# Optimization experiments

Hardware: AMD Instinct MI355X
Metric: run time of the kernel (lower is better)

Reference implementation:

```python
import jax, jax.numpy as jnp
import numpy as np

A_LO, A_HI = -1.0, 1.0  # arbitrary_range


def _kbit_gaussian(q_lo: float, q_hi: float, n_bit: int) -> jnp.ndarray:
    # torch: norm.ppf of quantiles 1/n..(n-1)/n, cast to fp16, then affine-normalize in fp16
    p = jnp.arange(1, n_bit, dtype=jnp.float32) / n_bit
    v = jax.scipy.stats.norm.ppf(p).astype(jnp.float16)
    return q_lo + (v - v[0]) / (v[-1] - v[0]) * (q_hi - q_lo)


def make_codebook() -> jnp.ndarray:
    neg = _kbit_gaussian(A_LO, 0.0, 2 ** 3)            # 7 values in [-1, 0]
    pos = _kbit_gaussian(0.0, A_HI, 2 ** 3 + 1)[1:]     # 8 values in (0, 1]
    return jnp.concatenate([neg, pos])                  # [15], float16


def setup_inputs() -> dict:
    key = jax.random.key(0)
    x = jax.random.normal(key, (2048, 4096), dtype=jnp.float32)
    codebook = make_codebook()
    return {"x": x, "codebook": codebook}


def reference(x, codebook):
    # fit: global min/max
    x_min = jnp.min(x)
    x_max = jnp.max(x)
    # fit_transform: clamp (no-op at fit min/max) + affine map to [A_LO, A_HI]
    x_norm = (jnp.clip(x, x_min, x_max) - x_min) / (x_max - x_min) * (A_HI - A_LO) + A_LO
    # nearest-codebook lookup: |x - c| argmin over 15-entry codebook, then gather
    dist = jnp.abs(x_norm[..., None] - codebook)  # [..., 15] (fp32, codebook upcast as in torch)
    idx = jnp.argmin(dist, axis=-1)
    return codebook[idx]  # float16, same shape as x
```

## Files before the change

### kernel.cpp

```cpp
#include <hip/hip_runtime.h>
#include <hip/hip_fp16.h>
#include <float.h>

#define N_CB 15
#define A_BLOCKS 512
#define A_THREADS 256
#define B_THREADS 256


__global__ __launch_bounds__(A_THREADS) void q4_partials_kernel(
        const float4* __restrict__ x4, int n4,
        const float* __restrict__ x, int n,
        float* __restrict__ ws, const void* __restrict__ cb_raw) {
    if (blockIdx.x == 0 && threadIdx.x < N_CB) {
        const float* cf = (const float*)cb_raw;
        float v;
        if (cf[0] == -1.0f) v = cf[threadIdx.x];
        else                v = __half2float(((const __half*)cb_raw)[threadIdx.x]);
        ws[1024 + threadIdx.x] = v;
    }

    float mn = FLT_MAX, mx = -FLT_MAX;
    int tid = blockIdx.x * A_THREADS + threadIdx.x;
    int stride = gridDim.x * A_THREADS;
    for (int i = tid; i < n4; i += stride) {
        float4 v = x4[i];
        mn = fminf(mn, fminf(fminf(v.x, v.y), fminf(v.z, v.w)));
        mx = fmaxf(mx, fmaxf(fmaxf(v.x, v.y), fmaxf(v.z, v.w)));
    }
    if (blockIdx.x == 0) {
        for (int i = n4 * 4 + threadIdx.x; i < n; i += A_THREADS) {
            float v = x[i];
            mn = fminf(mn, v);
            mx = fmaxf(mx, v);
        }
    }
    #pragma unroll
    for (int off = 32; off; off >>= 1) {
        mn = fminf(mn, __shfl_down(mn, off));
        mx = fmaxf(mx, __shfl_down(mx, off));
    }
    __shared__ float smn[4], smx[4];
    int wave = threadIdx.x >> 6, lane = threadIdx.x & 63;
    if (lane == 0) { smn[wave] = mn; smx[wave] = mx; }
    __syncthreads();
    if (threadIdx.x == 0) {
        ws[blockIdx.x]       = fminf(fminf(smn[0], smn[1]), fminf(smn[2], smn[3]));
        ws[512 + blockIdx.x] = fmaxf(fmaxf(smx[0], smx[1]), fmaxf(smx[2], smx[3]));
    }
}

__device__ __forceinline__ float q4_lookup(float xv, float mn, float range,
                                           const float* cb) {
    float t = (xv - mn) / range * 2.0f - 1.0f;
    float best = fabsf(t - cb[0]);
    float val  = cb[0];
    #pragma unroll
    for (int j = 1; j < N_CB; j++) {
        float d = fabsf(t - cb[j]);
        if (d < best) { best = d; val = cb[j]; }
    }
    return val;
}

__global__ __launch_bounds__(B_THREADS) void q4_transform_kernel(
        const float4* __restrict__ x4, float4* __restrict__ out4, int n4,
        const float* __restrict__ x, float* __restrict__ out, int n,
        const float* __restrict__ ws) {
    int base = blockIdx.x * (B_THREADS * 2) + threadIdx.x;
    bool h0 = base < n4, h1 = (base + B_THREADS) < n4;
    float4 v0, v1;
    if (h0) v0 = x4[base];
    if (h1) v1 = x4[base + B_THREADS];

    float mn = fminf(ws[threadIdx.x],       ws[threadIdx.x + 256]);
    float mx = fmaxf(ws[512 + threadIdx.x], ws[768 + threadIdx.x]);
    #pragma unroll
    for (int off = 32; off; off >>= 1) {
        mn = fminf(mn, __shfl_down(mn, off));
        mx = fmaxf(mx, __shfl_down(mx, off));
    }
    __shared__ float sred[8];
    __shared__ float sfin[2];
    int wave = threadIdx.x >> 6, lane = threadIdx.x & 63;
    if (lane == 0) { sred[wave] = mn; sred[4 + wave] = mx; }
    __syncthreads();
    if (threadIdx.x == 0) {
        sfin[0] = fminf(fminf(sred[0], sred[1]), fminf(sred[2], sred[3]));
        sfin[1] = fmaxf(fmaxf(sred[4], sred[5]), fmaxf(sred[6], sred[7]));
    }
    float cb[N_CB];
    #pragma unroll
    for (int j = 0; j < N_CB; j++) cb[j] = ws[1024 + j];
    __syncthreads();
    float fmn = sfin[0];
    float range = sfin[1] - fmn;

    if (h0) {
        float4 o;
        o.x = q4_lookup(v0.x, fmn, range, cb);
        o.y = q4_lookup(v0.y, fmn, range, cb);
        o.z = q4_lookup(v0.z, fmn, range, cb);
        o.w = q4_lookup(v0.w, fmn, range, cb);
        out4[base] = o;
    }
    if (h1) {
        float4 o;
        o.x = q4_lookup(v1.x, fmn, range, cb);
        o.y = q4_lookup(v1.y, fmn, range, cb);
        o.z = q4_lookup(v1.z, fmn, range, cb);
        o.w = q4_lookup(v1.w, fmn, range, cb);
        out4[base + B_THREADS] = o;
    }
    if (blockIdx.x == 0) {
        for (int k = n4 * 4 + threadIdx.x; k < n; k += B_THREADS) {
            out[k] = q4_lookup(x[k], fmn, range, cb);
        }
    }
}

extern "C" void kernel_launch(void* const* d_in, const int* in_sizes, int n_in,
                              void* d_out, int out_size, void* d_ws, size_t ws_size,
                              hipStream_t stream) {
    const float* x = (const float*)d_in[0];
    const void* cb = d_in[1];
    float* out = (float*)d_out;
    int n = in_sizes[0];
    int n4 = n >> 2;
    float* ws = (float*)d_ws;

    q4_partials_kernel<<<A_BLOCKS, A_THREADS, 0, stream>>>(
        (const float4*)x, n4, x, n, ws, cb);

    int bblocks = (n4 + B_THREADS * 2 - 1) / (B_THREADS * 2);
    q4_transform_kernel<<<bblocks, B_THREADS, 0, stream>>>(
        (const float4*)x, (float4*)out, n4, x, out, n, ws);
}
```

Measured before the change: 97.32 us.

## Fuse min/max reduction and quantize into one cooperative kernel with register-held tiles

Replaces the two-kernel flow (partial min/max, then transform) with a single cooperative persistent kernel. Each thread loads up to eight float4 values into registers, does the min/max reduction, meets the other blocks at a grid-wide sync, and then quantizes the values it already holds. This removes the second full read of x and one kernel launch. In exchange it adds a grid.sync, uses more registers per thread, and depends on cooperative launch support, with the old two-kernel path kept as a fallback.

```diff
diff --git a/kernel.cpp b/kernel.cpp
--- a/kernel.cpp
+++ b/kernel.cpp
@@ -1,54 +1,15 @@
 #include <hip/hip_runtime.h>
 #include <hip/hip_fp16.h>
+#include <hip/hip_cooperative_groups.h>
 #include <float.h>
 
-#define N_CB 15
-#define A_BLOCKS 512
-#define A_THREADS 256
-#define B_THREADS 256
-
-
-__global__ __launch_bounds__(A_THREADS) void q4_partials_kernel(
-        const float4* __restrict__ x4, int n4,
-        const float* __restrict__ x, int n,
-        float* __restrict__ ws, const void* __restrict__ cb_raw) {
-    if (blockIdx.x == 0 && threadIdx.x < N_CB) {
-        const float* cf = (const float*)cb_raw;
-        float v;
-        if (cf[0] == -1.0f) v = cf[threadIdx.x];
-        else                v = __half2float(((const __half*)cb_raw)[threadIdx.x]);
-        ws[1024 + threadIdx.x] = v;
-    }
-
-    float mn = FLT_MAX, mx = -FLT_MAX;
-    int tid = blockIdx.x * A_THREADS + threadIdx.x;
-    int stride = gridDim.x * A_THREADS;
-    for (int i = tid; i < n4; i += stride) {
-        float4 v = x4[i];
-        mn = fminf(mn, fminf(fminf(v.x, v.y), fminf(v.z, v.w)));
-        mx = fmaxf(mx, fmaxf(fmaxf(v.x, v.y), fmaxf(v.z, v.w)));
-    }
-    if (blockIdx.x == 0) {
-        for (int i = n4 * 4 + threadIdx.x; i < n; i += A_THREADS) {
-            float v = x[i];
-            mn = fminf(mn, v);
-            mx = fmaxf(mx, v);
-        }
-    }
-    #pragma unroll
-    for (int off = 32; off; off >>= 1) {
-        mn = fminf(mn, __shfl_down(mn, off));
-        mx = fmaxf(mx, __shfl_down(mx, off));
-    }
-    __shared__ float smn[4], smx[4];
-    int wave = threadIdx.x >> 6, lane = threadIdx.x & 63;
-    if (lane == 0) { smn[wave] = mn; smx[wave] = mx; }
-    __syncthreads();
-    if (threadIdx.x == 0) {
-        ws[blockIdx.x]       = fminf(fminf(smn[0], smn[1]), fminf(smn[2], smn[3]));
-        ws[512 + blockIdx.x] = fmaxf(fmaxf(smx[0], smx[1]), fmaxf(smx[2], smx[3]));
-    }
-}
+namespace cg = cooperative_groups;
+
+#define N_CB  15
+#define MAXB  1024
+#define NTHR  256
+#define VPT   8
+
 
 __device__ __forceinline__ float q4_lookup(float xv, float mn, float range,
                                            const float* cb) {
@@ -63,18 +24,170 @@
     return val;
 }
 
-__global__ __launch_bounds__(B_THREADS) void q4_transform_kernel(
+__device__ __forceinline__ void q4_load_cb(const void* __restrict__ cb_raw, float* cb) {
+    const float* cf = (const float*)cb_raw;
+    if (cf[0] == -1.0f) {
+        #pragma unroll
+        for (int j = 0; j < N_CB; j++) cb[j] = cf[j];
+    } else {
+        const __half* ch = (const __half*)cb_raw;
+        #pragma unroll
+        for (int j = 0; j < N_CB; j++) cb[j] = __half2float(ch[j]);
+    }
+}
+
+__global__ __launch_bounds__(NTHR, 4) void q4_fused_kernel(
+        const float4* __restrict__ x4, float4* __restrict__ out4, int n4,
+        const float* __restrict__ x, float* __restrict__ out, int n,
+        const void* __restrict__ cb_raw, float* __restrict__ ws) {
+    cg::grid_group grid = cg::this_grid();
+    const int g  = blockIdx.x * NTHR + threadIdx.x;
+    const int G  = gridDim.x * NTHR;
+    const int nb = gridDim.x;
+
+    float cb[N_CB];
+    q4_load_cb(cb_raw, cb);
+
+    float4 v[VPT];
+    bool   has[VPT];
+    float mn = FLT_MAX, mx = -FLT_MAX;
+    #pragma unroll
+    for (int j = 0; j < VPT; j++) {
+        int i = g + j * G;
+        has[j] = (i < n4);
+        if (has[j]) {
+            v[j] = x4[i];
+            mn = fminf(mn, fminf(fminf(v[j].x, v[j].y), fminf(v[j].z, v[j].w)));
+            mx = fmaxf(mx, fmaxf(fmaxf(v[j].x, v[j].y), fmaxf(v[j].z, v[j].w)));
+        }
+    }
+    for (int i = g + VPT * G; i < n4; i += G) {
+        float4 t = x4[i];
+        mn = fminf(mn, fminf(fminf(t.x, t.y), fminf(t.z, t.w)));
+        mx = fmaxf(mx, fmaxf(fmaxf(t.x, t.y), fmaxf(t.z, t.w)));
+    }
+    for (int i = n4 * 4 + g; i < n; i += G) {
+        float t = x[i];
+        mn = fminf(mn, t);
+        mx = fmaxf(mx, t);
+    }
+
+    #pragma unroll
+    for (int off = 32; off; off >>= 1) {
+        mn = fminf(mn, __shfl_down(mn, off));
+        mx = fmaxf(mx, __shfl_down(mx, off));
+    }
+    __shared__ float smn[4], smx[4];
+    __shared__ float sfin[2];
+    const int wave = threadIdx.x >> 6, lane = threadIdx.x & 63;
+    if (lane == 0) { smn[wave] = mn; smx[wave] = mx; }
+    __syncthreads();
+    if (threadIdx.x == 0) {
+        ws[blockIdx.x]        = fminf(fminf(smn[0], smn[1]), fminf(smn[2], smn[3]));
+        ws[MAXB + blockIdx.x] = fmaxf(fmaxf(smx[0], smx[1]), fmaxf(smx[2], smx[3]));
+    }
+
+    grid.sync();
+
+    mn = FLT_MAX; mx = -FLT_MAX;
+    for (int j = threadIdx.x; j < nb; j += NTHR) {
+        mn = fminf(mn, ws[j]);
+        mx = fmaxf(mx, ws[MAXB + j]);
+    }
+    #pragma unroll
+    for (int off = 32; off; off >>= 1) {
+        mn = fminf(mn, __shfl_down(mn, off));
+        mx = fmaxf(mx, __shfl_down(mx, off));
+    }
+    if (lane == 0) { smn[wave] = mn; smx[wave] = mx; }
+    __syncthreads();
+    if (threadIdx.x == 0) {
+        sfin[0] = fminf(fminf(smn[0], smn[1]), fminf(smn[2], smn[3]));
+        sfin[1] = fmaxf(fmaxf(smx[0], smx[1]), fmaxf(smx[2], smx[3]));
+    }
+    __syncthreads();
+    const float fmn   = sfin[0];
+    const float range = sfin[1] - fmn;
+
+    #pragma unroll
+    for (int j = 0; j < VPT; j++) {
+        if (has[j]) {
+            float4 o;
+            o.x = q4_lookup(v[j].x, fmn, range, cb);
+            o.y = q4_lookup(v[j].y, fmn, range, cb);
+            o.z = q4_lookup(v[j].z, fmn, range, cb);
+            o.w = q4_lookup(v[j].w, fmn, range, cb);
+            out4[g + j * G] = o;
+        }
+    }
+    for (int i = g + VPT * G; i < n4; i += G) {
+        float4 t = x4[i];
+        float4 o;
+        o.x = q4_lookup(t.x, fmn, range, cb);
+        o.y = q4_lookup(t.y, fmn, range, cb);
+        o.z = q4_lookup(t.z, fmn, range, cb);
+        o.w = q4_lookup(t.w, fmn, range, cb);
+        out4[i] = o;
+    }
+    for (int i = n4 * 4 + g; i < n; i += G) {
+        out[i] = q4_lookup(x[i], fmn, range, cb);
+    }
+}
+
+#define FB_OFF    4096
+#define FB_BLOCKS 512
+
+__global__ __launch_bounds__(NTHR) void q4_partials_kernel(
+        const float4* __restrict__ x4, int n4,
+        const float* __restrict__ x, int n,
+        float* __restrict__ ws, const void* __restrict__ cb_raw) {
+    if (blockIdx.x == 0 && threadIdx.x == 0) {
+        float cb[N_CB];
+        q4_load_cb(cb_raw, cb);
+        for (int j = 0; j < N_CB; j++) ws[FB_OFF + 1024 + j] = cb[j];
+    }
+    float mn = FLT_MAX, mx = -FLT_MAX;
+    int tid = blockIdx.x * NTHR + threadIdx.x;
+    int stride = gridDim.x * NTHR;
+    for (int i = tid; i < n4; i += stride) {
+        float4 v = x4[i];
+        mn = fminf(mn, fminf(fminf(v.x, v.y), fminf(v.z, v.w)));
+        mx = fmaxf(mx, fmaxf(fmaxf(v.x, v.y), fmaxf(v.z, v.w)));
+    }
+    if (blockIdx.x == 0) {
+        for (int i = n4 * 4 + threadIdx.x; i < n; i += NTHR) {
+            float v = x[i];
+            mn = fminf(mn, v);
+            mx = fmaxf(mx, v);
+        }
+    }
+    #pragma unroll
+    for (int off = 32; off; off >>= 1) {
+        mn = fminf(mn, __shfl_down(mn, off));
+        mx = fmaxf(mx, __shfl_down(mx, off));
+    }
+    __shared__ float smn[4], smx[4];
+    int wave = threadIdx.x >> 6, lane = threadIdx.x & 63;
+    if (lane == 0) { smn[wave] = mn; smx[wave] = mx; }
+    __syncthreads();
+    if (threadIdx.x == 0) {
+        ws[FB_OFF + blockIdx.x]       = fminf(fminf(smn[0], smn[1]), fminf(smn[2], smn[3]));
+        ws[FB_OFF + 512 + blockIdx.x] = fmaxf(fmaxf(smx[0], smx[1]), fmaxf(smx[2], smx[3]));
+    }
+}
+
+__global__ __launch_bounds__(NTHR) void q4_transform_kernel(
         const float4* __restrict__ x4, float4* __restrict__ out4, int n4,
         const float* __restrict__ x, float* __restrict__ out, int n,
         const float* __restrict__ ws) {
-    int base = blockIdx.x * (B_THREADS * 2) + threadIdx.x;
-    bool h0 = base < n4, h1 = (base + B_THREADS) < n4;
+    int base = blockIdx.x * (NTHR * 2) + threadIdx.x;
+    bool h0 = base < n4, h1 = (base + NTHR) < n4;
     float4 v0, v1;
     if (h0) v0 = x4[base];
-    if (h1) v1 = x4[base + B_THREADS];
-
-    float mn = fminf(ws[threadIdx.x],       ws[threadIdx.x + 256]);
-    float mx = fmaxf(ws[512 + threadIdx.x], ws[768 + threadIdx.x]);
+    if (h1) v1 = x4[base + NTHR];
+
+    float mn = fminf(ws[FB_OFF + threadIdx.x],       ws[FB_OFF + threadIdx.x + 256]);
+    float mx = fmaxf(ws[FB_OFF + 512 + threadIdx.x], ws[FB_OFF + 768 + threadIdx.x]);
     #pragma unroll
     for (int off = 32; off; off >>= 1) {
         mn = fminf(mn, __shfl_down(mn, off));
@@ -91,7 +204,7 @@
     }
     float cb[N_CB];
     #pragma unroll
-    for (int j = 0; j < N_CB; j++) cb[j] = ws[1024 + j];
+    for (int j = 0; j < N_CB; j++) cb[j] = ws[FB_OFF + 1024 + j];
     __syncthreads();
     float fmn = sfin[0];
     float range = sfin[1] - fmn;
@@ -110,10 +223,10 @@
         o.y = q4_lookup(v1.y, fmn, range, cb);
         o.z = q4_lookup(v1.z, fmn, range, cb);
         o.w = q4_lookup(v1.w, fmn, range, cb);
-        out4[base + B_THREADS] = o;
+        out4[base + NTHR] = o;
     }
     if (blockIdx.x == 0) {
-        for (int k = n4 * 4 + threadIdx.x; k < n; k += B_THREADS) {
+        for (int k = n4 * 4 + threadIdx.x; k < n; k += NTHR) {
             out[k] = q4_lookup(x[k], fmn, range, cb);
         }
     }
@@ -129,10 +242,29 @@
     int n4 = n >> 2;
     float* ws = (float*)d_ws;
 
-    q4_partials_kernel<<<A_BLOCKS, A_THREADS, 0, stream>>>(
-        (const float4*)x, n4, x, n, ws, cb);
-
-    int bblocks = (n4 + B_THREADS * 2 - 1) / (B_THREADS * 2);
-    q4_transform_kernel<<<bblocks, B_THREADS, 0, stream>>>(
-        (const float4*)x, (float4*)out, n4, x, out, n, ws);
-}
+    const float4* x4   = (const float4*)x;
+    float4*       out4 = (float4*)out;
+
+    int blocksPerCU = 0;
+    hipError_t qerr = hipOccupancyMaxActiveBlocksPerMultiprocessor(
+        &blocksPerCU, q4_fused_kernel, NTHR, 0);
+    int grid = 0;
+    if (qerr == hipSuccess && blocksPerCU > 0) {
+        grid = blocksPerCU * 256;
+        if (grid > MAXB) grid = MAXB;
+    }
+
+    hipError_t lerr = hipErrorUnknown;
+    if (grid > 0) {
+        void* args[] = { (void*)&x4, (void*)&out4, (void*)&n4,
+                         (void*)&x,  (void*)&out,  (void*)&n,
+                         (void*)&cb, (void*)&ws };
+        lerr = hipLaunchCooperativeKernel(q4_fused_kernel,
+                                          dim3(grid), dim3(NTHR), args, 0, stream);
+    }
+    if (lerr != hipSuccess) {
+        q4_partials_kernel<<<FB_BLOCKS, NTHR, 0, stream>>>(x4, n4, x, n, ws, cb);
+        int bblocks = (n4 + NTHR * 2 - 1) / (NTHR * 2);
+        q4_transform_kernel<<<bblocks, NTHR, 0, stream>>>(x4, out4, n4, x, out, n, ws);
+    }
+}
```

Result: slower. 148.8 us (+52.9%).
